# Kernel optimization log

Measured on AMD Instinct MI355X. Metric: run time of the kernel, lower is better.

Reference implementation:

```python
import jax, jax.numpy as jnp
import numpy as np


def _feature_vol(ref, tgt, maxdisp):
    """Vectorized diff cost volume.
    ref, tgt: [B, C, H, W]. Returns cost: [B, C, D, H, W] with
    cost[:, :, d, :, w] = |ref[:, :, :, w] - tgt[:, :, :, w-d]| for w >= d, else 0.
    Matches the torch loop: cost[:,:,i,:,i:] = |ref[:,:,:,i:] - tgt[:,:,:,:W-i]|.
    """
    B, C, H, W = ref.shape
    d = jnp.arange(maxdisp)[:, None]          # [D, 1]
    w = jnp.arange(W)[None, :]                # [1, W]
    idx = jnp.maximum(w - d, 0)               # [D, W] gather index into target width
    valid = (w >= d).astype(ref.dtype)        # [D, W]
    # gather shifted target: [B, C, H, D, W] -> [B, C, D, H, W]
    tgt_s = jnp.transpose(tgt[:, :, :, idx], (0, 1, 3, 2, 4))
    cost = jnp.abs(ref[:, :, None, :, :] - tgt_s) * valid[None, None, :, None, :]
    return cost


def setup_inputs() -> dict:
    key = jax.random.key(0)
    k1, k2 = jax.random.split(key)
    B, C, H, W = 4, 32, 80, 160
    refimg_fea = jax.random.normal(k1, (B, C, H, W), dtype=jnp.float32)
    targetimg_fea = jax.random.normal(k2, (B, C, H, W), dtype=jnp.float32)
    return {"refimg_fea": refimg_fea, "targetimg_fea": targetimg_fea, "maxdisp": 24}


def reference(refimg_fea, targetimg_fea, maxdisp):
    # diff cost volume [B, C, D, H, W]
    cost = _feature_vol(refimg_fea, targetimg_fea, maxdisp)
    # aggregate channels -> [B, D, H, W] (stand-in for the 3D decoder head's 1-ch output)
    cost_agg = cost.sum(axis=1)
    prob = jax.nn.softmax(cost_agg, axis=1)
    disp = jnp.arange(maxdisp, dtype=prob.dtype)
    pred = jnp.einsum('bdhw,d->bhw', prob, disp)  # [B, H, W]
    return pred
```

## Files before the change

kernel.cpp:

```cpp
#include <hip/hip_runtime.h>
#include <math.h>

#define BB 4
#define CC 32
#define HH 80
#define WW 160
#define DD 24

#define WT 32
#define NT (WW / WT)
#define HALO 23
#define SW (WT + HALO + 1)
#define NCG 8
#define CPG (CC / NCG)

__global__ __launch_bounds__(256) void hsm_fused_kernel(
    const float* __restrict__ ref,
    const float* __restrict__ tgt,
    float* __restrict__ out) {

    __shared__ float s_tgt[CC * SW];
    __shared__ float s_red[4 * DD * WT];

    const int blk  = blockIdx.x;
    const int tile = blk % NT;
    const int row  = blk / NT;
    const int b    = row / HH;
    const int h    = row % HH;
    const int w0   = tile * WT;
    const int tid  = threadIdx.x;
    const int wl   = tid & (WT - 1);
    const int cg   = tid >> 5;

    const float* tgt_row = tgt + ((size_t)b * CC * HH + h) * WW;
    for (int i = tid; i < CC * SW; i += 256) {
        const int c = i / SW;
        const int j = i - c * SW;
        const int gw = w0 - HALO + j;
        float v = 0.0f;
        if (gw >= 0 && gw < WW) v = tgt_row[(size_t)c * HH * WW + gw];
        s_tgt[i] = v;
    }
    __syncthreads();

    float acc[DD];
#pragma unroll
    for (int d = 0; d < DD; ++d) acc[d] = 0.0f;

    const float* ref_row = ref + ((size_t)b * CC * HH + h) * WW + w0 + wl;

    if (w0 != 0) {
#pragma unroll
        for (int cc = 0; cc < CPG; ++cc) {
            const int c = cg * CPG + cc;
            const float r = ref_row[(size_t)c * HH * WW];
            const float* t = &s_tgt[c * SW + HALO + wl];
#pragma unroll
            for (int d = 0; d < DD; ++d) {
                acc[d] += fabsf(r - t[-d]);
            }
        }
    } else {
#pragma unroll
        for (int cc = 0; cc < CPG; ++cc) {
            const int c = cg * CPG + cc;
            const float r = ref_row[(size_t)c * HH * WW];
            const float* t = &s_tgt[c * SW + HALO + wl];
#pragma unroll
            for (int d = 0; d < DD; ++d) {
                acc[d] += (d <= wl) ? fabsf(r - t[-d]) : 0.0f;
            }
        }
    }

#pragma unroll
    for (int half = 4; half >= 1; half >>= 1) {
        __syncthreads();
        if (cg >= half && cg < 2 * half) {
            const int rr = cg - half;
#pragma unroll
            for (int d = 0; d < DD; ++d) s_red[(rr * DD + d) * WT + wl] = acc[d];
        }
        __syncthreads();
        if (cg < half) {
#pragma unroll
            for (int d = 0; d < DD; ++d) acc[d] += s_red[(cg * DD + d) * WT + wl];
        }
    }

    if (cg == 0) {
        float m = acc[0];
#pragma unroll
        for (int d = 1; d < DD; ++d) m = fmaxf(m, acc[d]);
        float denom = 0.0f, num = 0.0f;
#pragma unroll
        for (int d = 0; d < DD; ++d) {
            const float e = __expf(acc[d] - m);
            denom += e;
            num += (float)d * e;
        }
        out[(size_t)row * WW + w0 + wl] = num / denom;
    }
}

extern "C" void kernel_launch(void* const* d_in, const int* in_sizes, int n_in,
                              void* d_out, int out_size, void* d_ws, size_t ws_size,
                              hipStream_t stream) {
    const float* ref = (const float*)d_in[0];
    const float* tgt = (const float*)d_in[1];
    float* out = (float*)d_out;

    hsm_fused_kernel<<<BB * HH * NT, 256, 0, stream>>>(ref, tgt, out);
}
```

Measured before the change: 78.23 us.

## Register-tile 4x4 disparity-width blocks with float4 shared loads and wider tiles

Reworks the fused cost-volume kernel so each thread computes a 4-disparity by 4-pixel register tile over half the channels, with vectorised float4 staging of both ref and tgt rows into shared memory. Width tiles grow to 64 (3 tiles per row, last partially masked) and blocks shrink to 192 threads. The multi-step tree reduction is replaced by a single two-way partial-sum merge. The aim is fewer shared loads per absolute difference and fewer barriers, at the cost of more idle lanes in the last tile and a fixed mapping tied to these sizes.

```diff
diff --git a/kernel.cpp b/kernel.cpp
--- a/kernel.cpp
+++ b/kernel.cpp
@@ -7,20 +7,21 @@
 #define WW 160
 #define DD 24
 
-#define WT 32
-#define NT (WW / WT)
-#define HALO 23
-#define SW (WT + HALO + 1)
-#define NCG 8
-#define CPG (CC / NCG)
+#define WT 64
+#define NT 3
+#define HALO 24
+#define SWW (WT + HALO)
+#define NDG 6
+#define NTH 192
 
-__global__ __launch_bounds__(256) void hsm_fused_kernel(
+__global__ __launch_bounds__(NTH) void hsm_fused_kernel(
     const float* __restrict__ ref,
     const float* __restrict__ tgt,
     float* __restrict__ out) {
 
-    __shared__ float s_tgt[CC * SW];
-    __shared__ float s_red[4 * DD * WT];
+    __shared__ __align__(16) float s_tgt[CC * SWW];
+    __shared__ __align__(16) float s_ref[CC * WT];
+    __shared__ __align__(16) float s_part[DD * WT];
 
     const int blk  = blockIdx.x;
     const int tile = blk % NT;
@@ -29,77 +30,113 @@
     const int h    = row % HH;
     const int w0   = tile * WT;
     const int tid  = threadIdx.x;
-    const int wl   = tid & (WT - 1);
-    const int cg   = tid >> 5;
+
+    const int w4 = tid & 15;
+    const int t2 = tid >> 4;
+    const int dg = t2 % NDG;
+    const int ch = t2 / NDG;
 
     const float* tgt_row = tgt + ((size_t)b * CC * HH + h) * WW;
-    for (int i = tid; i < CC * SW; i += 256) {
-        const int c = i / SW;
-        const int j = i - c * SW;
-        const int gw = w0 - HALO + j;
-        float v = 0.0f;
-        if (gw >= 0 && gw < WW) v = tgt_row[(size_t)c * HH * WW + gw];
-        s_tgt[i] = v;
+    const float* ref_row = ref + ((size_t)b * CC * HH + h) * WW;
+
+    for (int i = tid; i < CC * (SWW / 4); i += NTH) {
+        const int c  = i / (SWW / 4);
+        const int j4 = i - c * (SWW / 4);
+        const int gw = w0 - HALO + 4 * j4;
+        float4 v = make_float4(0.f, 0.f, 0.f, 0.f);
+        if (gw >= 0 && gw < WW) v = *(const float4*)(tgt_row + (size_t)c * HH * WW + gw);
+        *(float4*)&s_tgt[c * SWW + 4 * j4] = v;
+    }
+    for (int i = tid; i < CC * (WT / 4); i += NTH) {
+        const int c  = i >> 4;
+        const int j4 = i & 15;
+        const int gw = w0 + 4 * j4;
+        float4 v = make_float4(0.f, 0.f, 0.f, 0.f);
+        if (gw < WW) v = *(const float4*)(ref_row + (size_t)c * HH * WW + gw);
+        *(float4*)&s_ref[c * WT + 4 * j4] = v;
     }
     __syncthreads();
 
-    float acc[DD];
+    float acc[4][4];
 #pragma unroll
-    for (int d = 0; d < DD; ++d) acc[d] = 0.0f;
+    for (int k = 0; k < 4; ++k)
+#pragma unroll
+        for (int j = 0; j < 4; ++j) acc[k][j] = 0.0f;
 
-    const float* ref_row = ref + ((size_t)b * CC * HH + h) * WW + w0 + wl;
+    const int cbase = ch * (CC / 2);
+    const int tbase = 4 * (w4 - dg) + (HALO - 4);
 
     if (w0 != 0) {
+#pragma unroll 2
+        for (int cc = 0; cc < CC / 2; ++cc) {
+            const int c = cbase + cc;
+            const float4 r  = *(const float4*)&s_ref[c * WT + 4 * w4];
+            const float4 t0 = *(const float4*)&s_tgt[c * SWW + tbase];
+            const float4 t1 = *(const float4*)&s_tgt[c * SWW + tbase + 4];
+            const float rr[4] = {r.x, r.y, r.z, r.w};
+            const float w8[8] = {t0.x, t0.y, t0.z, t0.w, t1.x, t1.y, t1.z, t1.w};
 #pragma unroll
-        for (int cc = 0; cc < CPG; ++cc) {
-            const int c = cg * CPG + cc;
-            const float r = ref_row[(size_t)c * HH * WW];
-            const float* t = &s_tgt[c * SW + HALO + wl];
+            for (int k = 0; k < 4; ++k)
 #pragma unroll
-            for (int d = 0; d < DD; ++d) {
-                acc[d] += fabsf(r - t[-d]);
-            }
+                for (int j = 0; j < 4; ++j)
+                    acc[k][j] += fabsf(rr[j] - w8[j - k + 4]);
         }
     } else {
+#pragma unroll 2
+        for (int cc = 0; cc < CC / 2; ++cc) {
+            const int c = cbase + cc;
+            const float4 r  = *(const float4*)&s_ref[c * WT + 4 * w4];
+            const float4 t0 = *(const float4*)&s_tgt[c * SWW + tbase];
+            const float4 t1 = *(const float4*)&s_tgt[c * SWW + tbase + 4];
+            const float rr[4] = {r.x, r.y, r.z, r.w};
+            const float w8[8] = {t0.x, t0.y, t0.z, t0.w, t1.x, t1.y, t1.z, t1.w};
 #pragma unroll
-        for (int cc = 0; cc < CPG; ++cc) {
-            const int c = cg * CPG + cc;
-            const float r = ref_row[(size_t)c * HH * WW];
-            const float* t = &s_tgt[c * SW + HALO + wl];
+            for (int k = 0; k < 4; ++k)
 #pragma unroll
-            for (int d = 0; d < DD; ++d) {
-                acc[d] += (d <= wl) ? fabsf(r - t[-d]) : 0.0f;
-            }
+                for (int j = 0; j < 4; ++j)
+                    if (4 * w4 + j >= 4 * dg + k)
+                        acc[k][j] += fabsf(rr[j] - w8[j - k + 4]);
         }
     }
 
+    float4* part4 = (float4*)s_part;
+    if (ch == 1) {
 #pragma unroll
-    for (int half = 4; half >= 1; half >>= 1) {
-        __syncthreads();
-        if (cg >= half && cg < 2 * half) {
-            const int rr = cg - half;
-#pragma unroll
-            for (int d = 0; d < DD; ++d) s_red[(rr * DD + d) * WT + wl] = acc[d];
-        }
-        __syncthreads();
-        if (cg < half) {
-#pragma unroll
-            for (int d = 0; d < DD; ++d) acc[d] += s_red[(cg * DD + d) * WT + wl];
+        for (int k = 0; k < 4; ++k) {
+            const int d = 4 * dg + k;
+            part4[d * 16 + w4] = make_float4(acc[k][0], acc[k][1], acc[k][2], acc[k][3]);
         }
     }
+    __syncthreads();
+    if (ch == 0) {
+#pragma unroll
+        for (int k = 0; k < 4; ++k) {
+            const int d = 4 * dg + k;
+            float4 p = part4[d * 16 + w4];
+            p.x += acc[k][0]; p.y += acc[k][1]; p.z += acc[k][2]; p.w += acc[k][3];
+            part4[d * 16 + w4] = p;
+        }
+    }
+    __syncthreads();
 
-    if (cg == 0) {
-        float m = acc[0];
+    if (tid < WT) {
+        const int w = w0 + tid;
+        if (w < WW) {
+            float a[DD];
 #pragma unroll
-        for (int d = 1; d < DD; ++d) m = fmaxf(m, acc[d]);
-        float denom = 0.0f, num = 0.0f;
+            for (int d = 0; d < DD; ++d) a[d] = s_part[d * WT + tid];
+            float m = a[0];
 #pragma unroll
-        for (int d = 0; d < DD; ++d) {
-            const float e = __expf(acc[d] - m);
-            denom += e;
-            num += (float)d * e;
+            for (int d = 1; d < DD; ++d) m = fmaxf(m, a[d]);
+            float denom = 0.0f, num = 0.0f;
+#pragma unroll
+            for (int d = 0; d < DD; ++d) {
+                const float e = __expf(a[d] - m);
+                denom += e;
+                num += (float)d * e;
+            }
+            out[(size_t)row * WW + w] = num / denom;
         }
-        out[(size_t)row * WW + w0 + wl] = num / denom;
     }
 }
 
@@ -110,5 +147,5 @@
     const float* tgt = (const float*)d_in[1];
     float* out = (float*)d_out;
 
-    hsm_fused_kernel<<<BB * HH * NT, 256, 0, stream>>>(ref, tgt, out);
+    hsm_fused_kernel<<<BB * HH * NT, NTH, 0, stream>>>(ref, tgt, out);
 }
```

Measured after the change: 70.39 us. -10.0%, faster.
